# Performance work log

Measured on AMD Instinct MI355X. Metric: run time of the kernel, lower is better.

Reference implementation:

```python
import jax, jax.numpy as jnp
import numpy as np

B, N, D = 8, 512, 1024
E, H, TOP_K = 8, 8, 2
HD = D // H
EPS = 1e-5


def setup_inputs() -> dict:
    key = jax.random.key(0)
    ks = jax.random.split(key, 8)
    # kaiming_uniform with a=sqrt(5) over fan_in=N -> bound = sqrt(6/((1+5)*N)) = 1/sqrt(N)
    bound_w = 1.0 / np.sqrt(N)
    bound_lin = 1.0 / np.sqrt(D)
    return {
        "x": jax.random.normal(ks[0], (B, N, D), dtype=jnp.float32),
        "weight": jax.random.uniform(ks[1], (E, H, N, N), jnp.float32, -bound_w, bound_w),
        "bias": jnp.zeros((E, H, N), jnp.float32),
        "router_w": jax.random.uniform(ks[2], (E, D), jnp.float32, -bound_lin, bound_lin),
        "in_w": jax.random.uniform(ks[3], (D, D), jnp.float32, -bound_lin, bound_lin),
        "in_b": jax.random.uniform(ks[4], (D,), jnp.float32, -bound_lin, bound_lin),
        "out_w": jax.random.uniform(ks[5], (D, D), jnp.float32, -bound_lin, bound_lin),
        "out_b": jax.random.uniform(ks[6], (D,), jnp.float32, -bound_lin, bound_lin),
    }


def reference(x, weight, bias, router_w, in_w, in_b, out_w, out_b):
    # Router: mean-pool tokens, linear, softmax, top-k
    router_logits = x.mean(axis=1) @ router_w.T              # (B, E)
    router_probs = jax.nn.softmax(router_logits, axis=-1)
    top_w, top_i = jax.lax.top_k(router_probs, TOP_K)        # (B, K)
    top_w = top_w / top_w.sum(axis=-1, keepdims=True)

    # Input projection -> (B, H, hd, N), layer-norm over token axis N (no affine)
    xp = x @ in_w.T + in_b                                   # (B, N, D)
    xr = xp.reshape(B, N, H, HD).transpose(0, 2, 3, 1)       # (B, H, hd, N)
    mu = xr.mean(axis=-1, keepdims=True)
    var = xr.var(axis=-1, keepdims=True)
    xn = (xr - mu) * jax.lax.rsqrt(var + EPS)

    # Gather per-(batch, head, k) NxN expert matrices, row-softmax
    w = weight[top_i].transpose(0, 2, 1, 3, 4)               # (B, H, K, N, N)
    b = bias[top_i].transpose(0, 2, 1, 3)                    # (B, H, K, N)
    w_attn = jax.nn.softmax(w, axis=-1)

    # out[b,h,k,d,m] = sum_n xn[b,h,d,n] * w_attn[b,h,k,m,n]
    out = jnp.einsum('bhdn,bhkmn->bhkdm', xn, w_attn)
    out = out + b[:, :, :, None, :]                          # (B, H, K, hd, N)
    out = (out * top_w[:, None, :, None, None]).sum(axis=2)  # (B, H, hd, N)

    out = out.transpose(0, 3, 1, 2).reshape(B, N, D)         # (B, N, D)
    out = out @ out_w.T + out_b

    # Load-balancing aux loss
    top1 = top_i[:, 0]
    expert_mask = jax.nn.one_hot(top1, E, dtype=jnp.float32)
    aux = E * (router_probs.mean(axis=0) * expert_mask.mean(axis=0)).sum()
    return out, aux
```

## Files before the change

kernel.cpp:

```cpp
#include <hip/hip_runtime.h>
#include <hip/hip_bf16.h>

#define Bv 8
#define Nv 512
#define Dv 1024
#define Ev 8
#define Hv 8
#define HDv 128
#define EPSv 1e-5f

typedef __attribute__((ext_vector_type(8))) short short8;
typedef __attribute__((ext_vector_type(4))) float f32x4;

__device__ __forceinline__ unsigned short f2b(float f) {
    __hip_bfloat16 h = __float2bfloat16(f);
    return *reinterpret_cast<unsigned short*>(&h);
}
__device__ __forceinline__ float bf2f(unsigned int u) {
    union { unsigned int i; float f; } v; v.i = u << 16; return v.f;
}
__device__ __forceinline__ unsigned int blend2(unsigned int a, unsigned int b,
                                               float tw0, float tw1) {
    float lo = tw0 * bf2f(a & 0xffffu) + tw1 * bf2f(b & 0xffffu);
    float hi = tw0 * bf2f(a >> 16)     + tw1 * bf2f(b >> 16);
    return (unsigned int)f2b(lo) | ((unsigned int)f2b(hi) << 16);
}

__device__ __forceinline__ void gld16(const void* g, void* l) {
    __builtin_amdgcn_global_load_lds(
        (const __attribute__((address_space(1))) void*)(uintptr_t)(g),
        (__attribute__((address_space(3))) void*)(uintptr_t)(l), 16, 0, 0);
}

__global__ __launch_bounds__(256) void k_pre(const float* __restrict__ x,
                                             const float* __restrict__ weight,
                                             const float* __restrict__ w1,
                                             const float* __restrict__ w2,
                                             unsigned short* __restrict__ xb,
                                             float* __restrict__ part_x,
                                             unsigned short* __restrict__ wa,
                                             unsigned short* __restrict__ w1b,
                                             unsigned short* __restrict__ w2b) {
    int bid = blockIdx.x;
    int t = threadIdx.x;
    if (bid < 128) {
        int b = bid >> 4, c = bid & 15;
        const float* px = x + ((size_t)b * Nv + c * 32) * Dv + t * 4;
        unsigned short* qx = xb + ((size_t)b * Nv + c * 32) * Dv + t * 4;
        float4 s4 = make_float4(0.f, 0.f, 0.f, 0.f);
        #pragma unroll 8
        for (int r = 0; r < 32; ++r) {
            float4 v = *(const float4*)(px + (size_t)r * Dv);
            s4.x += v.x; s4.y += v.y; s4.z += v.z; s4.w += v.w;
            uint2 pk;
            pk.x = (unsigned)f2b(v.x) | ((unsigned)f2b(v.y) << 16);
            pk.y = (unsigned)f2b(v.z) | ((unsigned)f2b(v.w) << 16);
            *(uint2*)(qx + (size_t)r * Dv) = pk;
        }
        *(float4*)(part_x + ((size_t)(b * 16 + c)) * Dv + t * 4) = s4;
        return;
    }
    if (bid < 1152) {
        int lane = t & 63;
        int r0 = ((bid - 128) * 4 + (t >> 6)) * 8;
        const float* wp = weight + (size_t)r0 * Nv + lane * 8;
        float v[8][8];
        #pragma unroll
        for (int r = 0; r < 8; ++r) {
            float4 a = *(const float4*)(wp + (size_t)r * Nv);
            float4 b = *(const float4*)(wp + (size_t)r * Nv + 4);
            v[r][0] = a.x; v[r][1] = a.y; v[r][2] = a.z; v[r][3] = a.w;
            v[r][4] = b.x; v[r][5] = b.y; v[r][6] = b.z; v[r][7] = b.w;
        }
        float sm[8];
        #pragma unroll
        for (int r = 0; r < 8; ++r) {
            #pragma unroll
            for (int i = 0; i < 8; ++i) v[r][i] = __expf(v[r][i]);
            float s01 = v[r][0] + v[r][1], s23 = v[r][2] + v[r][3];
            float s45 = v[r][4] + v[r][5], s67 = v[r][6] + v[r][7];
            sm[r] = (s01 + s23) + (s45 + s67);
        }
        for (int off = 1; off < 64; off <<= 1) {
            #pragma unroll
            for (int r = 0; r < 8; ++r) sm[r] += __shfl_xor(sm[r], off);
        }
        #pragma unroll
        for (int r = 0; r < 8; ++r) {
            float inv = 1.f / sm[r];
            uint4 pk;
            pk.x = (unsigned)f2b(v[r][0] * inv) | ((unsigned)f2b(v[r][1] * inv) << 16);
            pk.y = (unsigned)f2b(v[r][2] * inv) | ((unsigned)f2b(v[r][3] * inv) << 16);
            pk.z = (unsigned)f2b(v[r][4] * inv) | ((unsigned)f2b(v[r][5] * inv) << 16);
            pk.w = (unsigned)f2b(v[r][6] * inv) | ((unsigned)f2b(v[r][7] * inv) << 16);
            *(uint4*)(wa + (size_t)(r0 + r) * Nv + lane * 8) = pk;
        }
        return;
    }
    int c = (bid - 1152) * 256 + t;
    const float* src; unsigned short* dst; int off;
    if (c < 131072) { src = w1; dst = w1b; off = c; }
    else            { src = w2; dst = w2b; off = c - 131072; }
    float4 a = ((const float4*)src)[off * 2];
    float4 b = ((const float4*)src)[off * 2 + 1];
    union { unsigned short h[8]; uint4 u; } pk;
    pk.h[0] = f2b(a.x); pk.h[1] = f2b(a.y); pk.h[2] = f2b(a.z); pk.h[3] = f2b(a.w);
    pk.h[4] = f2b(b.x); pk.h[5] = f2b(b.y); pk.h[6] = f2b(b.z); pk.h[7] = f2b(b.w);
    ((uint4*)dst)[off] = pk.u;
}

template <int MODE>
__global__ __launch_bounds__(256) void k_gemm(
    const unsigned short* __restrict__ A,
    const unsigned short* __restrict__ W,
    const float* __restrict__ bias,
    void* __restrict__ Cv,
    float2* __restrict__ part,
    const float* __restrict__ part_x,
    float* __restrict__ xmean,
    int M, int Nn, int K) {
    __shared__ __align__(16) unsigned short sA[3][128 * 64];
    __shared__ __align__(16) unsigned short sB[3][128 * 64];
    const int t = threadIdx.x;
    const int bn = blockIdx.x * 128;
    const int bm = blockIdx.y * 128;
    const int lane = t & 63;
    const int w = t >> 6, wm = w >> 1, wn = w & 1;
    const int fr = lane & 15, fq = lane >> 4;
    const int NT = K >> 6;
    f32x4 acc[4][4] = {};

#define STAGE(s, k0)                                                        \
    {                                                                       \
        _Pragma("unroll")                                                   \
        for (int i_ = 0; i_ < 4; ++i_) {                                    \
            int c_ = t + i_ * 256;                                          \
            int row_ = c_ >> 3, col_ = c_ & 7;                              \
            int cs_ = col_ ^ (row_ & 7);                                    \
            gld16(A + (size_t)(bm + row_) * K + (k0) + cs_ * 8, &sA[s][c_ * 8]); \
            gld16(W + (size_t)(bn + row_) * K + (k0) + cs_ * 8, &sB[s][c_ * 8]); \
        }                                                                   \
    }

    STAGE(0, 0);
    STAGE(1, 64);
    if (MODE == 2) {
        int blk = blockIdx.y * 8 + blockIdx.x;
        int o = blk * 32 + (t >> 3);
        int c2 = t & 7;
        int b2 = o >> 10, d2 = o & 1023;
        float S = part_x[((size_t)(b2 * 16 + c2)) * Dv + d2]
                + part_x[((size_t)(b2 * 16 + c2 + 8)) * Dv + d2];
        S += __shfl_xor(S, 1); S += __shfl_xor(S, 2); S += __shfl_xor(S, 4);
        if (c2 == 0) xmean[o] = S * (1.f / Nv);
    }
    for (int it = 0; it < NT; ++it) {
        if (it + 2 < NT) {
            STAGE((it + 2) % 3, (it + 2) * 64);
            asm volatile("s_waitcnt vmcnt(16)" ::: "memory");
        } else if (it + 1 < NT) {
            asm volatile("s_waitcnt vmcnt(8)" ::: "memory");
        } else {
            asm volatile("s_waitcnt vmcnt(0)" ::: "memory");
        }
        __builtin_amdgcn_s_barrier();
        const unsigned short* pA = sA[it % 3];
        const unsigned short* pB = sB[it % 3];
        #pragma unroll
        for (int kk = 0; kk < 2; ++kk) {
            short8 af[4], bv[4];
            #pragma unroll
            for (int i = 0; i < 4; ++i)
                af[i] = *(const short8*)&pA[(wm * 64 + i * 16 + fr) * 64 + (((kk << 2) + fq) ^ (fr & 7)) * 8];
            #pragma unroll
            for (int j = 0; j < 4; ++j)
                bv[j] = *(const short8*)&pB[(wn * 64 + j * 16 + fr) * 64 + (((kk << 2) + fq) ^ (fr & 7)) * 8];
            #pragma unroll
            for (int i = 0; i < 4; ++i)
                #pragma unroll
                for (int j = 0; j < 4; ++j)
                    acc[i][j] = __builtin_amdgcn_mfma_f32_16x16x32_bf16(af[i], bv[j], acc[i][j], 0, 0, 0);
        }
        __builtin_amdgcn_s_barrier();
    }
#undef STAGE
    if (MODE == 0) {
        #pragma unroll
        for (int j = 0; j < 4; ++j) {
            const int n = bn + wn * 64 + j * 16 + fr;
            const float bj = bias[n];
            #pragma unroll
            for (int i = 0; i < 4; ++i) {
                const int m0 = bm + wm * 64 + i * 16 + fq * 4;
                #pragma unroll
                for (int r = 0; r < 4; ++r)
                    ((float*)Cv)[(size_t)(m0 + r) * Nn + n] = acc[i][j][r] + bj;
            }
        }
    } else {
        unsigned short* sc = &sA[0][0];
        float2* red = (float2*)&sB[0][0];
        const int bB   = bm >> 9;
        const int tok0 = bm & 511;
        const int chunk = (bm >> 7) & 3;
        #pragma unroll
        for (int j = 0; j < 4; ++j) {
            const int col = wn * 64 + j * 16 + fr;
            const float bj = bias[bn + col];
            float s = 0.f, q = 0.f;
            #pragma unroll
            for (int i = 0; i < 4; ++i) {
                const int row0 = wm * 64 + i * 16 + fq * 4;
                #pragma unroll
                for (int r = 0; r < 4; r += 2) {
                    float v0 = acc[i][j][r] + bj;
                    float v1 = acc[i][j][r + 1] + bj;
                    s += v0 + v1;
                    q = fmaf(v0, v0, fmaf(v1, v1, q));
                    unsigned int pk = (unsigned int)f2b(v0) | ((unsigned int)f2b(v1) << 16);
                    *(unsigned int*)&sc[col * 136 + row0 + r] = pk;
                }
            }
            red[col * 8 + wm * 4 + fq] = make_float2(s, q);
        }
        __syncthreads();
        if (t < 128) {
            float S = 0.f, Q = 0.f;
            #pragma unroll
            for (int k = 0; k < 8; ++k) { float2 v = red[t * 8 + k]; S += v.x; Q += v.y; }
            part[((size_t)bB * Dv + bn + t) * 4 + chunk] = make_float2(S, Q);
        }
        unsigned short* dst = (unsigned short*)Cv;
        #pragma unroll
        for (int k = 0; k < 8; ++k) {
            const int c = t + k * 256;
            const int dl = c >> 4, tk = c & 15;
            uint4 v = *(const uint4*)&sc[dl * 136 + tk * 8];
            *(uint4*)&dst[((size_t)bB * Dv + bn + dl) * Nv + tok0 + tk * 8] = v;
        }
    }
}

__global__ __launch_bounds__(256) void k_mixg(
    const unsigned short* __restrict__ wa,
    const unsigned short* __restrict__ xpT,
    const float* __restrict__ bias,
    const float* __restrict__ xmean,
    const float* __restrict__ router_w,
    const float2* __restrict__ part,
    unsigned short* __restrict__ y,
    float* __restrict__ aux_out) {
    __shared__ __align__(16) unsigned short sA[2][128 * 64];
    __shared__ __align__(16) unsigned short sB[2][128 * 64];
    __shared__ float probs[Bv][Ev];
    __shared__ float twsh[Bv][2];
    __shared__ int   tsel[Bv][2];
    __shared__ int   top1s[Bv];
    const int t = threadIdx.x;
    const int bm = blockIdx.x * 128;
    const int bh = blockIdx.y;
    const int b = bh >> 3, h = bh & 7;

    {
        int pid = t >> 2, l = t & 3;
        int rb = pid >> 3, re = pid & 7;
        const float4* xm = (const float4*)(xmean + rb * Dv);
        const float4* rw = (const float4*)(router_w + re * Dv);
        float s = 0.f;
        #pragma unroll
        for (int j = 0; j < 64; ++j) {
            float4 aa = xm[l + j * 4], ww = rw[l + j * 4];
            s = fmaf(aa.x, ww.x, s); s = fmaf(aa.y, ww.y, s);
            s = fmaf(aa.z, ww.z, s); s = fmaf(aa.w, ww.w, s);
        }
        s += __shfl_xor(s, 1); s += __shfl_xor(s, 2);
        if (l == 0) probs[rb][re] = s;
    }
    __syncthreads();
    if (t < Bv) {
        int bb = t;
        float mx = -1e30f;
        for (int e2 = 0; e2 < Ev; ++e2) mx = fmaxf(mx, probs[bb][e2]);
        float sum = 0.f;
        for (int e2 = 0; e2 < Ev; ++e2) { float v = __expf(probs[bb][e2] - mx); probs[bb][e2] = v; sum += v; }
        float inv = 1.f / sum;
        for (int e2 = 0; e2 < Ev; ++e2) probs[bb][e2] *= inv;
        int i0 = 0; float p0 = probs[bb][0];
        for (int e2 = 1; e2 < Ev; ++e2) if (probs[bb][e2] > p0) { p0 = probs[bb][e2]; i0 = e2; }
        int i1 = -1; float p1 = -1.f;
        for (int e2 = 0; e2 < Ev; ++e2) if (e2 != i0 && probs[bb][e2] > p1) { p1 = probs[bb][e2]; i1 = e2; }
        float s2 = p0 + p1;
        tsel[bb][0] = i0; tsel[bb][1] = i1;
        twsh[bb][0] = p0 / s2; twsh[bb][1] = p1 / s2;
        top1s[bb] = i0;
    }
    __syncthreads();
    if (blockIdx.x == 0 && bh == 0 && t == 0) {
        float aux = 0.f;
        for (int e2 = 0; e2 < Ev; ++e2) {
            float pm = 0.f, mm = 0.f;
            for (int bb = 0; bb < Bv; ++bb) { pm += probs[bb][e2]; mm += (top1s[bb] == e2) ? 1.f : 0.f; }
            aux += (pm / Bv) * (mm / Bv);
        }
        *aux_out = aux * Ev;
    }
    const int e0 = tsel[b][0], e1 = tsel[b][1];
    const float tw0 = twsh[b][0], tw1 = twsh[b][1];

    const int lane = t & 63;
    const int w = t >> 6, wm = w >> 1, wn = w & 1;
    const int fr = lane & 15, fq = lane >> 4;

    float rstd_j[4], nmr_j[4];
    #pragma unroll
    for (int j = 0; j < 4; ++j) {
        const int dg = h * HDv + wn * 64 + j * 16 + fr;
        const float2* pp = part + ((size_t)b * Dv + dg) * 4;
        float S = 0.f, Q = 0.f;
        #pragma unroll
        for (int cc = 0; cc < 4; ++cc) { float2 v = pp[cc]; S += v.x; Q += v.y; }
        float mu = S * (1.f / Nv);
        float var = Q * (1.f / Nv) - mu * mu;
        float rs = rsqrtf(var + EPSv);
        rstd_j[j] = rs; nmr_j[j] = -mu * rs;
    }

    const unsigned short* A0 = wa + (size_t)(e0 * Hv + h) * Nv * Nv;
    const unsigned short* A1 = wa + (size_t)(e1 * Hv + h) * Nv * Nv;
    const unsigned short* Bb = xpT + ((size_t)b * Dv + h * HDv) * Nv;
    const int NT = Nv >> 6;
    f32x4 acc[4][4] = {};
    uint4 ra0[4], ra1[4];

#define BSTAGE(s, k0)                                                       \
    {                                                                       \
        _Pragma("unroll")                                                   \
        for (int i_ = 0; i_ < 4; ++i_) {                                    \
            int c_ = t + i_ * 256;                                          \
            int row_ = c_ >> 3, col_ = c_ & 7;                              \
            int cs_ = col_ ^ (row_ & 7);                                    \
            gld16(Bb + (size_t)row_ * Nv + (k0) + cs_ * 8, &sB[s][c_ * 8]); \
        }                                                                   \
    }
#define ALOAD(k0)                                                           \
    {                                                                       \
        _Pragma("unroll")                                                   \
        for (int i_ = 0; i_ < 4; ++i_) {                                    \
            int c_ = t + i_ * 256;                                          \
            int row_ = c_ >> 3, col_ = c_ & 7;                              \
            int cs_ = col_ ^ (row_ & 7);                                    \
            size_t off_ = (size_t)(bm + row_) * Nv + (k0) + cs_ * 8;        \
            ra0[i_] = *(const uint4*)&A0[off_];                             \
            ra1[i_] = *(const uint4*)&A1[off_];                             \
        }                                                                   \
    }

    BSTAGE(0, 0);
    ALOAD(0);
    for (int it = 0; it < NT; ++it) {
        if (it + 1 < NT) {
            BSTAGE((it + 1) & 1, (it + 1) * 64);
            asm volatile("s_waitcnt vmcnt(4)" ::: "memory");
        } else {
            asm volatile("s_waitcnt vmcnt(0)" ::: "memory");
        }
        #pragma unroll
        for (int i = 0; i < 4; ++i) {
            int c = t + i * 256;
            uint4 o;
            o.x = blend2(ra0[i].x, ra1[i].x, tw0, tw1);
            o.y = blend2(ra0[i].y, ra1[i].y, tw0, tw1);
            o.z = blend2(ra0[i].z, ra1[i].z, tw0, tw1);
            o.w = blend2(ra0[i].w, ra1[i].w, tw0, tw1);
            *(uint4*)&sA[it & 1][c * 8] = o;
        }
        if (it + 1 < NT) ALOAD((it + 1) * 64);
        asm volatile("s_waitcnt lgkmcnt(0)" ::: "memory");
        __builtin_amdgcn_s_barrier();
        const unsigned short* pA = sA[it & 1];
        const unsigned short* pB = sB[it & 1];
        #pragma unroll
        for (int kk = 0; kk < 2; ++kk) {
            short8 af[4], bv[4];
            #pragma unroll
            for (int i = 0; i < 4; ++i)
                af[i] = *(const short8*)&pA[(wm * 64 + i * 16 + fr) * 64 + (((kk << 2) + fq) ^ (fr & 7)) * 8];
            #pragma unroll
            for (int j = 0; j < 4; ++j)
                bv[j] = *(const short8*)&pB[(wn * 64 + j * 16 + fr) * 64 + (((kk << 2) + fq) ^ (fr & 7)) * 8];
            #pragma unroll
            for (int i = 0; i < 4; ++i)
                #pragma unroll
                for (int j = 0; j < 4; ++j)
                    acc[i][j] = __builtin_amdgcn_mfma_f32_16x16x32_bf16(af[i], bv[j], acc[i][j], 0, 0, 0);
        }
        __builtin_amdgcn_s_barrier();
    }
#undef BSTAGE
#undef ALOAD
    #pragma unroll
    for (int i = 0; i < 4; ++i) {
        #pragma unroll
        for (int r = 0; r < 4; ++r) {
            const int m = bm + wm * 64 + i * 16 + fq * 4 + r;
            const float br = tw0 * bias[(size_t)(e0 * Hv + h) * Nv + m]
                           + tw1 * bias[(size_t)(e1 * Hv + h) * Nv + m];
            #pragma unroll
            for (int j = 0; j < 4; ++j) {
                const int d = wn * 64 + j * 16 + fr;
                float v = fmaf(acc[i][j][r], rstd_j[j], nmr_j[j] + br);
                y[((size_t)b * Nv + m) * Dv + h * HDv + d] = f2b(v);
            }
        }
    }
}

extern "C" void kernel_launch(void* const* d_in, const int* in_sizes, int n_in,
                              void* d_out, int out_size, void* d_ws, size_t ws_size,
                              hipStream_t stream) {
    const float* x        = (const float*)d_in[0];
    const float* weight   = (const float*)d_in[1];
    const float* bias     = (const float*)d_in[2];
    const float* router_w = (const float*)d_in[3];
    const float* in_w     = (const float*)d_in[4];
    const float* in_b     = (const float*)d_in[5];
    const float* out_w    = (const float*)d_in[6];
    const float* out_b    = (const float*)d_in[7];
    float* out = (float*)d_out;

    if (ws_size < ((size_t)63 << 20)) return;

    char* wsb = (char*)d_ws;
    float*  xmean  = (float*)(wsb);
    float2* part   = (float2*)(wsb + (64 << 10));
    float*  part_x = (float*)(wsb + (512 << 10));
    unsigned short* in_wb  = (unsigned short*)(wsb + ((size_t)2 << 20));
    unsigned short* out_wb = (unsigned short*)(wsb + ((size_t)4 << 20));
    unsigned short* xb     = (unsigned short*)(wsb + ((size_t)8 << 20));
    unsigned short* xpT    = (unsigned short*)(wsb + ((size_t)16 << 20));
    unsigned short* wa     = (unsigned short*)(wsb + ((size_t)24 << 20));
    unsigned short* y = xb;

    k_pre<<<2176, 256, 0, stream>>>(x, weight, in_w, out_w, xb, part_x, wa, in_wb, out_wb);
    k_gemm<2><<<dim3(8, 32), 256, 0, stream>>>(xb, in_wb, in_b, xpT, part, part_x, xmean,
                                               Bv * Nv, Dv, Dv);
    k_mixg<<<dim3(4, 64), 256, 0, stream>>>(wa, xpT, bias, xmean, router_w, part, y,
                                            out + (size_t)Bv * Nv * Dv);
    k_gemm<0><<<dim3(8, 32), 256, 0, stream>>>(y, out_wb, out_b, out, nullptr, nullptr, nullptr,
                                               Bv * Nv, Dv, Dv);
}
```

Baseline: 75.98 us.

## Fuse expert-weight softmax into input-projection GEMM main loop

Moves the row-softmax and bf16 conversion of the expert weight tensor out of the preprocessing kernel and into the MODE 2 input-projection GEMM, interleaving the global loads and exp/reduce work with the MFMA pipeline. The aim is to hide the memory-bound weight-softmax pass under the compute-bound GEMM and shrink the pre kernel's grid. In exchange it adds register pressure (two 16-float prefetch buffers), retuned vmcnt waits, and an extra barrier before the epilogue, which could lower occupancy or stall the MFMA pipeline.

```diff
diff --git a/kernel.cpp b/kernel.cpp
--- a/kernel.cpp
+++ b/kernel.cpp
@@ -33,12 +33,10 @@
 }
 
 __global__ __launch_bounds__(256) void k_pre(const float* __restrict__ x,
-                                             const float* __restrict__ weight,
                                              const float* __restrict__ w1,
                                              const float* __restrict__ w2,
                                              unsigned short* __restrict__ xb,
                                              float* __restrict__ part_x,
-                                             unsigned short* __restrict__ wa,
                                              unsigned short* __restrict__ w1b,
                                              unsigned short* __restrict__ w2b) {
     int bid = blockIdx.x;
@@ -60,44 +58,7 @@
         *(float4*)(part_x + ((size_t)(b * 16 + c)) * Dv + t * 4) = s4;
         return;
     }
-    if (bid < 1152) {
-        int lane = t & 63;
-        int r0 = ((bid - 128) * 4 + (t >> 6)) * 8;
-        const float* wp = weight + (size_t)r0 * Nv + lane * 8;
-        float v[8][8];
-        #pragma unroll
-        for (int r = 0; r < 8; ++r) {
-            float4 a = *(const float4*)(wp + (size_t)r * Nv);
-            float4 b = *(const float4*)(wp + (size_t)r * Nv + 4);
-            v[r][0] = a.x; v[r][1] = a.y; v[r][2] = a.z; v[r][3] = a.w;
-            v[r][4] = b.x; v[r][5] = b.y; v[r][6] = b.z; v[r][7] = b.w;
-        }
-        float sm[8];
-        #pragma unroll
-        for (int r = 0; r < 8; ++r) {
-            #pragma unroll
-            for (int i = 0; i < 8; ++i) v[r][i] = __expf(v[r][i]);
-            float s01 = v[r][0] + v[r][1], s23 = v[r][2] + v[r][3];
-            float s45 = v[r][4] + v[r][5], s67 = v[r][6] + v[r][7];
-            sm[r] = (s01 + s23) + (s45 + s67);
-        }
-        for (int off = 1; off < 64; off <<= 1) {
-            #pragma unroll
-            for (int r = 0; r < 8; ++r) sm[r] += __shfl_xor(sm[r], off);
-        }
-        #pragma unroll
-        for (int r = 0; r < 8; ++r) {
-            float inv = 1.f / sm[r];
-            uint4 pk;
-            pk.x = (unsigned)f2b(v[r][0] * inv) | ((unsigned)f2b(v[r][1] * inv) << 16);
-            pk.y = (unsigned)f2b(v[r][2] * inv) | ((unsigned)f2b(v[r][3] * inv) << 16);
-            pk.z = (unsigned)f2b(v[r][4] * inv) | ((unsigned)f2b(v[r][5] * inv) << 16);
-            pk.w = (unsigned)f2b(v[r][6] * inv) | ((unsigned)f2b(v[r][7] * inv) << 16);
-            *(uint4*)(wa + (size_t)(r0 + r) * Nv + lane * 8) = pk;
-        }
-        return;
-    }
-    int c = (bid - 1152) * 256 + t;
+    int c = (bid - 128) * 256 + t;
     const float* src; unsigned short* dst; int off;
     if (c < 131072) { src = w1; dst = w1b; off = c; }
     else            { src = w2; dst = w2b; off = c - 131072; }
@@ -118,6 +79,8 @@
     float2* __restrict__ part,
     const float* __restrict__ part_x,
     float* __restrict__ xmean,
+    const float* __restrict__ wsrc,
+    unsigned short* __restrict__ wa_out,
     int M, int Nn, int K) {
     __shared__ __align__(16) unsigned short sA[3][128 * 64];
     __shared__ __align__(16) unsigned short sB[3][128 * 64];
@@ -127,7 +90,7 @@
     const int lane = t & 63;
     const int w = t >> 6, wm = w >> 1, wn = w & 1;
     const int fr = lane & 15, fq = lane >> 4;
-    const int NT = K >> 6;
+    const int NT = (MODE == 2) ? 16 : (K >> 6);
     f32x4 acc[4][4] = {};
 
 #define STAGE(s, k0)                                                        \
@@ -142,48 +105,126 @@
         }                                                                   \
     }
 
-    STAGE(0, 0);
-    STAGE(1, 64);
+#define MFMA_PHASE(sidx)                                                    \
+    {                                                                       \
+        const unsigned short* pA = sA[sidx];                                \
+        const unsigned short* pB = sB[sidx];                                \
+        _Pragma("unroll")                                                   \
+        for (int kk = 0; kk < 2; ++kk) {                                    \
+            short8 af[4], bv[4];                                            \
+            _Pragma("unroll")                                               \
+            for (int i = 0; i < 4; ++i)                                     \
+                af[i] = *(const short8*)&pA[(wm * 64 + i * 16 + fr) * 64 + (((kk << 2) + fq) ^ (fr & 7)) * 8]; \
+            _Pragma("unroll")                                               \
+            for (int j = 0; j < 4; ++j)                                     \
+                bv[j] = *(const short8*)&pB[(wn * 64 + j * 16 + fr) * 64 + (((kk << 2) + fq) ^ (fr & 7)) * 8]; \
+            _Pragma("unroll")                                               \
+            for (int i = 0; i < 4; ++i)                                     \
+                _Pragma("unroll")                                           \
+                for (int j = 0; j < 4; ++j)                                 \
+                    acc[i][j] = __builtin_amdgcn_mfma_f32_16x16x32_bf16(af[i], bv[j], acc[i][j], 0, 0, 0); \
+        }                                                                   \
+    }
+
     if (MODE == 2) {
-        int blk = blockIdx.y * 8 + blockIdx.x;
+        const int blk = blockIdx.y * 8 + blockIdx.x;
+        const int rwbase = blk * 128 + (t >> 6) * 2;
+        float ga[16], gb[16];
+
+#define GLOAD(DST, g)                                                       \
+    {                                                                       \
+        const float* p_ = wsrc + (size_t)(rwbase + (g) * 8) * 512 + lane * 8; \
+        float4 a_ = *(const float4*)p_;                                     \
+        float4 b_ = *(const float4*)(p_ + 4);                               \
+        float4 c_ = *(const float4*)(p_ + 512);                             \
+        float4 d_ = *(const float4*)(p_ + 516);                             \
+        DST[0] = a_.x; DST[1] = a_.y; DST[2] = a_.z; DST[3] = a_.w;         \
+        DST[4] = b_.x; DST[5] = b_.y; DST[6] = b_.z; DST[7] = b_.w;         \
+        DST[8] = c_.x; DST[9] = c_.y; DST[10] = c_.z; DST[11] = c_.w;       \
+        DST[12] = d_.x; DST[13] = d_.y; DST[14] = d_.z; DST[15] = d_.w;     \
+    }
+
+#define CONSUME(SRC, g)                                                     \
+    {                                                                       \
+        float e_[16];                                                       \
+        _Pragma("unroll")                                                   \
+        for (int q_ = 0; q_ < 16; ++q_) e_[q_] = __expf(SRC[q_]);           \
+        float s0_ = ((e_[0] + e_[1]) + (e_[2] + e_[3])) + ((e_[4] + e_[5]) + (e_[6] + e_[7])); \
+        float s1_ = ((e_[8] + e_[9]) + (e_[10] + e_[11])) + ((e_[12] + e_[13]) + (e_[14] + e_[15])); \
+        for (int off_ = 1; off_ < 64; off_ <<= 1) {                         \
+            s0_ += __shfl_xor(s0_, off_);                                   \
+            s1_ += __shfl_xor(s1_, off_);                                   \
+        }                                                                   \
+        float i0_ = 1.f / s0_, i1_ = 1.f / s1_;                             \
+        uint4 p0_, p1_;                                                     \
+        p0_.x = (unsigned)f2b(e_[0] * i0_) | ((unsigned)f2b(e_[1] * i0_) << 16); \
+        p0_.y = (unsigned)f2b(e_[2] * i0_) | ((unsigned)f2b(e_[3] * i0_) << 16); \
+        p0_.z = (unsigned)f2b(e_[4] * i0_) | ((unsigned)f2b(e_[5] * i0_) << 16); \
+        p0_.w = (unsigned)f2b(e_[6] * i0_) | ((unsigned)f2b(e_[7] * i0_) << 16); \
+        p1_.x = (unsigned)f2b(e_[8] * i1_) | ((unsigned)f2b(e_[9] * i1_) << 16); \
+        p1_.y = (unsigned)f2b(e_[10] * i1_) | ((unsigned)f2b(e_[11] * i1_) << 16); \
+        p1_.z = (unsigned)f2b(e_[12] * i1_) | ((unsigned)f2b(e_[13] * i1_) << 16); \
+        p1_.w = (unsigned)f2b(e_[14] * i1_) | ((unsigned)f2b(e_[15] * i1_) << 16); \
+        unsigned short* wp_ = wa_out + (size_t)(rwbase + (g) * 8) * 512 + lane * 8; \
+        *(uint4*)wp_ = p0_;                                                 \
+        *(uint4*)(wp_ + 512) = p1_;                                         \
+    }
+
+#define FITER(it, CUR, NXT)                                                 \
+    {                                                                       \
+        if ((it) + 2 < 16) STAGE(((it) + 2) % 3, ((it) + 2) * 64);          \
+        if ((it) + 1 < 16) GLOAD(NXT, (it) + 1);                            \
+        if ((it) + 2 < 16) {                                                \
+            asm volatile("s_waitcnt vmcnt(14)" ::: "memory");               \
+        } else if ((it) + 1 < 16) {                                         \
+            asm volatile("s_waitcnt vmcnt(6)" ::: "memory");                \
+        } else {                                                            \
+            asm volatile("s_waitcnt vmcnt(2)" ::: "memory");                \
+        }                                                                   \
+        __builtin_amdgcn_s_barrier();                                       \
+        MFMA_PHASE((it) % 3);                                               \
+        CONSUME(CUR, (it));                                                 \
+        __builtin_amdgcn_s_barrier();                                       \
+    }
+
         int o = blk * 32 + (t >> 3);
         int c2 = t & 7;
         int b2 = o >> 10, d2 = o & 1023;
         float S = part_x[((size_t)(b2 * 16 + c2)) * Dv + d2]
                 + part_x[((size_t)(b2 * 16 + c2 + 8)) * Dv + d2];
+        STAGE(0, 0);
+        STAGE(1, 64);
+        GLOAD(ga, 0);
         S += __shfl_xor(S, 1); S += __shfl_xor(S, 2); S += __shfl_xor(S, 4);
         if (c2 == 0) xmean[o] = S * (1.f / Nv);
-    }
-    for (int it = 0; it < NT; ++it) {
-        if (it + 2 < NT) {
-            STAGE((it + 2) % 3, (it + 2) * 64);
-            asm volatile("s_waitcnt vmcnt(16)" ::: "memory");
-        } else if (it + 1 < NT) {
-            asm volatile("s_waitcnt vmcnt(8)" ::: "memory");
-        } else {
-            asm volatile("s_waitcnt vmcnt(0)" ::: "memory");
-        }
-        __builtin_amdgcn_s_barrier();
-        const unsigned short* pA = sA[it % 3];
-        const unsigned short* pB = sB[it % 3];
-        #pragma unroll
-        for (int kk = 0; kk < 2; ++kk) {
-            short8 af[4], bv[4];
-            #pragma unroll
-            for (int i = 0; i < 4; ++i)
-                af[i] = *(const short8*)&pA[(wm * 64 + i * 16 + fr) * 64 + (((kk << 2) + fq) ^ (fr & 7)) * 8];
-            #pragma unroll
-            for (int j = 0; j < 4; ++j)
-                bv[j] = *(const short8*)&pB[(wn * 64 + j * 16 + fr) * 64 + (((kk << 2) + fq) ^ (fr & 7)) * 8];
-            #pragma unroll
-            for (int i = 0; i < 4; ++i)
-                #pragma unroll
-                for (int j = 0; j < 4; ++j)
-                    acc[i][j] = __builtin_amdgcn_mfma_f32_16x16x32_bf16(af[i], bv[j], acc[i][j], 0, 0, 0);
-        }
-        __builtin_amdgcn_s_barrier();
+
+        for (int it2 = 0; it2 < 16; it2 += 2) {
+            FITER(it2, ga, gb);
+            FITER(it2 + 1, gb, ga);
+        }
+#undef FITER
+#undef CONSUME
+#undef GLOAD
+    } else {
+        STAGE(0, 0);
+        STAGE(1, 64);
+        for (int it = 0; it < NT; ++it) {
+            if (it + 2 < NT) {
+                STAGE((it + 2) % 3, (it + 2) * 64);
+                asm volatile("s_waitcnt vmcnt(16)" ::: "memory");
+            } else if (it + 1 < NT) {
+                asm volatile("s_waitcnt vmcnt(8)" ::: "memory");
+            } else {
+                asm volatile("s_waitcnt vmcnt(0)" ::: "memory");
+            }
+            __builtin_amdgcn_s_barrier();
+            MFMA_PHASE(it % 3);
+            __builtin_amdgcn_s_barrier();
+        }
     }
 #undef STAGE
+#undef MFMA_PHASE
+
     if (MODE == 0) {
         #pragma unroll
         for (int j = 0; j < 4; ++j) {
@@ -203,6 +244,7 @@
         const int bB   = bm >> 9;
         const int tok0 = bm & 511;
         const int chunk = (bm >> 7) & 3;
+        __syncthreads();
         #pragma unroll
         for (int j = 0; j < 4; ++j) {
             const int col = wn * 64 + j * 16 + fr;
@@ -441,11 +483,11 @@
     unsigned short* wa     = (unsigned short*)(wsb + ((size_t)24 << 20));
     unsigned short* y = xb;
 
-    k_pre<<<2176, 256, 0, stream>>>(x, weight, in_w, out_w, xb, part_x, wa, in_wb, out_wb);
+    k_pre<<<1152, 256, 0, stream>>>(x, in_w, out_w, xb, part_x, in_wb, out_wb);
     k_gemm<2><<<dim3(8, 32), 256, 0, stream>>>(xb, in_wb, in_b, xpT, part, part_x, xmean,
-                                               Bv * Nv, Dv, Dv);
+                                               weight, wa, Bv * Nv, Dv, Dv);
     k_mixg<<<dim3(4, 64), 256, 0, stream>>>(wa, xpT, bias, xmean, router_w, part, y,
                                             out + (size_t)Bv * Nv * Dv);
     k_gemm<0><<<dim3(8, 32), 256, 0, stream>>>(y, out_wb, out_b, out, nullptr, nullptr, nullptr,
-                                               Bv * Nv, Dv, Dv);
-}
+                                               nullptr, nullptr, Bv * Nv, Dv, Dv);
+}
```

New measurement: 79.41 us. 4.5% more time.
